# Optimization experiments

Measured on AMD Instinct MI355X. Metric: run time of the kernel, lower is better.

## Reference

```python
import jax, jax.numpy as jnp
import numpy as np

IMG_W, IMG_H = 960.0, 512.0   # image_size (w, h)
HM_W, HM_H = 240, 128         # heatmap_size (w, h)


def _bilinear(fmap, gx, gy):
    # fmap: [C,H,W]; gx, gy: [N] normalized coords; bilinear, align_corners=False, zero padding
    C, H, W = fmap.shape
    ix = (gx + 1.0) * W * 0.5 - 0.5
    iy = (gy + 1.0) * H * 0.5 - 0.5
    x0f = jnp.floor(ix); y0f = jnp.floor(iy)
    wx1 = ix - x0f; wy1 = iy - y0f

    def tap(xf, yf, wgt):
        valid = (xf >= 0) & (xf <= W - 1) & (yf >= 0) & (yf <= H - 1)
        xc = jnp.clip(xf.astype(jnp.int32), 0, W - 1)
        yc = jnp.clip(yf.astype(jnp.int32), 0, H - 1)
        return fmap[:, yc, xc] * (wgt * valid.astype(fmap.dtype))

    return (tap(x0f, y0f, (1 - wx1) * (1 - wy1)) + tap(x0f + 1, y0f, wx1 * (1 - wy1))
            + tap(x0f, y0f + 1, (1 - wx1) * wy1) + tap(x0f + 1, y0f + 1, wx1 * wy1))


def _forward(feature_maps, grid_center, space_center, space_size, sub_space_size,
             cube, centers, trans, cam_R, cam_T, cam_f, cam_c):
    n_cam, B, C, H, W = feature_maps.shape
    vox = jnp.float32(cube)
    fine_n = (space_size / sub_space_size * (vox - 1.0)).astype(jnp.int32) + 1   # [3]
    fine_nf = fine_n.astype(jnp.float32)
    scale = (fine_nf - 1.0) / space_size
    bias = (-sub_space_size / 2.0 / space_size * (fine_nf - 1.0)
            - scale * (space_center - space_size / 2.0))
    centers_tl = jnp.round(grid_center[:, :3] * scale + bias).astype(jnp.int32)  # [B,3]
    offset = (centers_tl.astype(jnp.float32) / (fine_nf - 1.0) * space_size
              - space_size / 2.0 + sub_space_size / 2.0)                          # [B,3]
    mask_xy = jnp.maximum(((1.0 - grid_center[:, 5:7]) / 2.0 * (vox - 1.0)).astype(jnp.int32), 0)
    mask = jnp.concatenate([mask_xy, jnp.zeros((B, 1), jnp.int32)], axis=1)       # [B,3]
    start = jnp.maximum(centers_tl + mask, 0)
    end = jnp.minimum(centers_tl + cube - mask, fine_n)
    end = jnp.maximum(end, start + 1)

    # fixed-size sub-cube of fine-grid indices; out-of-window cells are masked to 0
    v = jnp.arange(cube)
    mesh = jnp.stack(jnp.meshgrid(v, v, v, indexing="ij"), axis=-1).reshape(-1, 3)  # [N,3]
    fidx = centers_tl[:, None, :] + mesh[None]                                       # [B,N,3]
    valid = jnp.all((fidx >= start[:, None, :]) & (fidx < end[:, None, :]), axis=-1)  # [B,N]
    valid = valid & (grid_center[:, 3:4] >= 0)
    world = (space_center - space_size / 2.0
             + fidx.astype(jnp.float32) / (fine_nf - 1.0) * space_size)              # [B,N,3]

    # pinhole world->pixel per (batch, camera)
    rel = world[:, None, :, :] - cam_T[:, :, None, :]                                # [B,K,N,3]
    Xc = jnp.einsum("bkij,bknj->bkni", cam_R, rel)
    xy = cam_f[:, :, None, :] * Xc[..., :2] / Xc[..., 2:3] + cam_c[:, :, None, :]    # [B,K,N,2]
    maxwh = jnp.max(centers * 2.0, axis=-1)[:, :, None, None]
    xy = jnp.clip(xy, -1.0, maxwh)
    xy = jnp.einsum("bkij,bknj->bkni", trans[..., :2], xy) + trans[:, :, None, :, 2]  # affine crop
    xy = xy * jnp.array([HM_W / IMG_W, HM_H / IMG_H], jnp.float32)
    g = jnp.clip(xy / jnp.array([HM_W - 1.0, HM_H - 1.0], jnp.float32) * 2.0 - 1.0, -1.1, 1.1)

    fm = jnp.transpose(feature_maps, (1, 0, 2, 3, 4))                                # [B,K,C,H,W]
    samp = jax.vmap(jax.vmap(_bilinear))(fm, g[..., 0], g[..., 1])                   # [B,K,C,N]
    samp = samp * valid[:, None, None, :].astype(samp.dtype)
    cubes = jnp.sum(samp, axis=1) / (n_cam + 1e-6)            # mean agg (bounding==1)
    cubes = jnp.clip(cubes, 0.0, 1.0).reshape(B, C, cube, cube, cube)
    return cubes, offset


def setup_inputs() -> dict:
    key = jax.random.key(0)
    ks = jax.random.split(key, 10)
    n_cam, B, C, H, W = 5, 4, 15, 128, 240
    feature_maps = jax.random.uniform(ks[0], (n_cam, B, C, H, W), jnp.float32)
    xy = jax.random.uniform(ks[1], (B, 2), minval=-3000.0, maxval=3000.0)
    z = jax.random.uniform(ks[2], (B, 1), minval=800.0, maxval=1200.0)
    flag = jnp.ones((B, 2), jnp.float32)  # cols 3 (validity >= 0) and 4
    m = jax.random.uniform(ks[3], (B, 2), minval=0.6, maxval=1.0)  # cols 5:7 mask fracs
    grid_center = jnp.concatenate([xy, z, flag, m], axis=1)        # [B,7]
    space_center = jnp.array([0.0, 0.0, 1000.0], jnp.float32)
    space_size = jnp.array([8000.0, 8000.0, 2000.0], jnp.float32)
    sub_space_size = jnp.array([2000.0, 2000.0, 2000.0], jnp.float32)
    centers = jnp.array([IMG_W / 2, IMG_H / 2], jnp.float32) + \
        jax.random.uniform(ks[4], (B, n_cam, 2), minval=-5.0, maxval=5.0)
    base = jnp.array([[1.0, 0.0, 0.0], [0.0, 1.0, 0.0]], jnp.float32)
    trans = base + 0.01 * jax.random.normal(ks[5], (B, n_cam, 2, 3), jnp.float32)
    cam_R = jnp.eye(3, dtype=jnp.float32) + 0.05 * jax.random.normal(ks[6], (B, n_cam, 3, 3), jnp.float32)
    t_xy = jax.random.uniform(ks[7], (B, n_cam, 2), minval=-500.0, maxval=500.0)
    cam_T = jnp.concatenate([t_xy, jnp.full((B, n_cam, 1), -6000.0, jnp.float32)], axis=-1)
    cam_f = jax.random.uniform(ks[8], (B, n_cam, 2), minval=500.0, maxval=700.0)
    cam_c = jnp.array([IMG_W / 2, IMG_H / 2], jnp.float32) + \
        jax.random.uniform(ks[9], (B, n_cam, 2), minval=-10.0, maxval=10.0)
    return {"feature_maps": feature_maps, "grid_center": grid_center,
            "space_center": space_center, "space_size": space_size,
            "sub_space_size": sub_space_size, "sub_cube_size": 64,
            "centers": centers, "trans": trans, "cam_R": cam_R,
            "cam_T": cam_T, "cam_f": cam_f, "cam_c": cam_c}


def reference(feature_maps, grid_center, space_center, space_size, sub_space_size,
              sub_cube_size, centers, trans, cam_R, cam_T, cam_f, cam_c):
    return _forward(feature_maps, grid_center, space_center, space_size, sub_space_size,
                    int(sub_cube_size), centers, trans, cam_R, cam_T, cam_f, cam_c)
```

## Files before the change

### kernel.cpp

```cpp
#include <hip/hip_runtime.h>
#include <hip/hip_fp16.h>

#define NCAM 5
#define NC 15
#define NCP 16
#define FH 128
#define FW 240
#define HW (FH*FW)
#define CUBE 64
#define NVOX (CUBE*CUBE*CUBE)
#define MTHREADS 512
#define MBLOCKS_PER_B (NVOX/MTHREADS)
#define TTHREADS 256
#define CSTR 24

__global__ __launch_bounds__(TTHREADS) void transpose_fm(
    const float* __restrict__ fm, __half* __restrict__ fmH,
    const float* __restrict__ gc, const float* __restrict__ space_c,
    const float* __restrict__ space_s, const float* __restrict__ sub_s,
    const float* __restrict__ centers, const float* __restrict__ trans,
    const float* __restrict__ cam_R, const float* __restrict__ cam_T,
    const float* __restrict__ cam_f, const float* __restrict__ cam_c,
    float* __restrict__ camS, int* __restrict__ bwin,
    float* __restrict__ out, int B)
{
    const int t = threadIdx.x;
    if (blockIdx.x == 0 && blockIdx.y == 0) {
        if (t < B) {
            const int b = t;
            #pragma unroll
            for (int d = 0; d < 3; ++d) {
                float ssz = space_s[d], sc = space_c[d], sub = sub_s[d];
                int   fn  = (int)(ssz / sub * (CUBE - 1.0f)) + 1;
                float fnf = (float)fn;
                float scale = (fnf - 1.0f) / ssz;
                float bias  = -sub / 2.0f / ssz * (fnf - 1.0f) - scale * (sc - ssz / 2.0f);
                int ctl = (int)rintf(gc[b*7 + d] * scale + bias);
                int mask = 0;
                if (d < 2) {
                    mask = (int)((1.0f - gc[b*7 + 5 + d]) / 2.0f * (CUBE - 1.0f));
                    if (mask < 0) mask = 0;
                }
                int st = max(ctl + mask, 0);
                int en = min(ctl + CUBE - mask, fn);
                en = max(en, st + 1);
                bwin[b*12 + d]     = ctl;
                bwin[b*12 + 3 + d] = st;
                bwin[b*12 + 6 + d] = en;
                out[(size_t)B * NC * NVOX + b*3 + d] =
                    (float)ctl / (fnf - 1.0f) * ssz - ssz / 2.0f + sub / 2.0f;
            }
            bwin[t*12 + 9] = (gc[t*7 + 3] >= 0.0f) ? 1 : 0;
        }
        if (t < B * NCAM) {
            const int b = t / NCAM, bk = t;
            float sA[3], bA[3];
            #pragma unroll
            for (int d = 0; d < 3; ++d) {
                float ssz = space_s[d], sub = sub_s[d];
                int   fn  = (int)(ssz / sub * (CUBE - 1.0f)) + 1;
                sA[d] = ssz / ((float)fn - 1.0f);
                bA[d] = space_c[d] - ssz * 0.5f;
            }
            const float* R = cam_R + bk*9;
            const float* T = cam_T + bk*3;
            float* P = camS + (size_t)bk * CSTR;
            #pragma unroll
            for (int i = 0; i < 3; ++i) {
                #pragma unroll
                for (int d = 0; d < 3; ++d) P[i*3 + d] = R[i*3 + d] * sA[d];
                P[9 + i] = R[i*3+0]*(bA[0]-T[0]) + R[i*3+1]*(bA[1]-T[1]) + R[i*3+2]*(bA[2]-T[2]);
            }
            P[12] = cam_f[bk*2+0];  P[13] = cam_f[bk*2+1];
            P[14] = cam_c[bk*2+0];  P[15] = cam_c[bk*2+1];
            P[16] = fmaxf(centers[bk*2+0]*2.0f, centers[bk*2+1]*2.0f);
            const float* tr = trans + bk*6;
            const float KX = 60.0f/239.0f, KY = 32.0f/127.0f;
            P[17] = tr[0]*KX;  P[18] = tr[1]*KX;  P[19] = tr[2]*KX - 120.0f;
            P[20] = tr[3]*KY;  P[21] = tr[4]*KY;  P[22] = tr[5]*KY - 64.0f;
            P[23] = 0.0f;
            (void)b;
        }
    }
    const int p  = blockIdx.x * TTHREADS + t;
    const int cb = blockIdx.y;
    const float* src = fm + (size_t)cb * NC * HW + p;
    __half v[NCP];
    #pragma unroll
    for (int c = 0; c < NC; ++c) v[c] = __float2half(src[(size_t)c * HW]);
    v[15] = __float2half(0.0f);
    uint4* dst = (uint4*)(fmH + ((size_t)cb * HW + p) * NCP);
    dst[0] = *(const uint4*)(v);
    dst[1] = *(const uint4*)(v + 8);
}

#define FMA_MIX2(lo, hi, wt, wrd)                                             \
    asm("v_fma_mix_f32 %0, %1, %2, %0 op_sel_hi:[0,1,0]"                      \
        : "+v"(lo) : "v"(wt), "v"(wrd));                                      \
    asm("v_fma_mix_f32 %0, %1, %2, %0 op_sel:[0,1,0] op_sel_hi:[0,1,0]"       \
        : "+v"(hi) : "v"(wt), "v"(wrd));

#define TAPFMA(wt, A, Bv)                                                     \
    FMA_MIX2(acc[0],  acc[1],  wt, A.x)                                       \
    FMA_MIX2(acc[2],  acc[3],  wt, A.y)                                       \
    FMA_MIX2(acc[4],  acc[5],  wt, A.z)                                       \
    FMA_MIX2(acc[6],  acc[7],  wt, A.w)                                       \
    FMA_MIX2(acc[8],  acc[9],  wt, Bv.x)                                      \
    FMA_MIX2(acc[10], acc[11], wt, Bv.y)                                      \
    FMA_MIX2(acc[12], acc[13], wt, Bv.z)                                      \
    FMA_MIX2(acc[14], acc[15], wt, Bv.w)

struct CamProj { unsigned o[4]; float w[4]; };

__device__ __forceinline__ CamProj projcam(const float* __restrict__ P,
                                           float fxf, float fyf, float fzf)
{
    float X0 = fmaf(P[0], fxf, fmaf(P[1], fyf, fmaf(P[2], fzf, P[9])));
    float X1 = fmaf(P[3], fxf, fmaf(P[4], fyf, fmaf(P[5], fzf, P[10])));
    float X2 = fmaf(P[6], fxf, fmaf(P[7], fyf, fmaf(P[8], fzf, P[11])));
    float rz = __builtin_amdgcn_rcpf(X2);
    float mw = P[16];
    float px = fmaf(P[12]*X0, rz, P[14]);
    float py = fmaf(P[13]*X1, rz, P[15]);
    px = fminf(fmaxf(px, -1.0f), mw);
    py = fminf(fmaxf(py, -1.0f), mw);
    float ixf = fminf(fmaxf(fmaf(P[17], px, fmaf(P[18], py, P[19])), -132.0f), 132.0f) + 119.5f;
    float iyf = fminf(fmaxf(fmaf(P[20], px, fmaf(P[21], py, P[22])), -70.4f), 70.4f) + 63.5f;
    float x0f = floorf(ixf), y0f = floorf(iyf);
    float wx1 = ixf - x0f,  wy1 = iyf - y0f;
    float wx0 = 1.0f - wx1, wy0 = 1.0f - wy1;
    int x0 = (int)x0f, y0 = (int)y0f, x1 = x0 + 1, y1 = y0 + 1;
    bool vx0 = (unsigned)x0 <= (FW-1), vx1 = (unsigned)x1 <= (FW-1);
    bool vy0 = (unsigned)y0 <= (FH-1), vy1 = (unsigned)y1 <= (FH-1);
    CamProj r;
    r.w[0] = (vx0 && vy0) ? wx0*wy0 : 0.0f;
    r.w[1] = (vx1 && vy0) ? wx1*wy0 : 0.0f;
    r.w[2] = (vx0 && vy1) ? wx0*wy1 : 0.0f;
    r.w[3] = (vx1 && vy1) ? wx1*wy1 : 0.0f;
    int xc0 = min(max(x0,0),FW-1), xc1 = min(max(x1,0),FW-1);
    int yc0 = min(max(y0,0),FH-1), yc1 = min(max(y1,0),FH-1);
    r.o[0] = (unsigned)(yc0*FW + xc0);  r.o[1] = (unsigned)(yc0*FW + xc1);
    r.o[2] = (unsigned)(yc1*FW + xc0);  r.o[3] = (unsigned)(yc1*FW + xc1);
    return r;
}

__global__ __launch_bounds__(MTHREADS) void proj_main(
    const __half* __restrict__ fmH,
    const float* __restrict__ camS,
    const int* __restrict__ bwin,
    float* __restrict__ out, int B)
{
    const int b = blockIdx.x / MBLOCKS_PER_B;
    const int n = (blockIdx.x % MBLOCKS_PER_B) * MTHREADS + threadIdx.x;
    const int vi = n >> 12, vj = (n >> 6) & 63, vk = n & 63;

    const int* W = bwin + b*12;
    const int fx = W[0] + vi, fy = W[1] + vj, fz = W[2] + vk;
    const bool valid = (fx >= W[3]) & (fx < W[6])
                     & (fy >= W[4]) & (fy < W[7])
                     & (fz >= W[5]) & (fz < W[8])
                     & (W[9] != 0);

    float acc[NCP];
    #pragma unroll
    for (int c = 0; c < NCP; ++c) acc[c] = 0.0f;

    if (valid) {
        const float fxf = (float)fx, fyf = (float)fy, fzf = (float)fz;
        const float* cs = camS + (size_t)(b*NCAM) * CSTR;

        #pragma unroll
        for (int cam = 0; cam < NCAM; ++cam) {
            CamProj cp = projcam(cs + cam*CSTR, fxf, fyf, fzf);
            if (__any((cp.w[0] + cp.w[1] + cp.w[2] + cp.w[3]) != 0.0f)) {
                const __half* bp = fmH + (size_t)(cam*B + b) * HW * NCP;
                const uint4* q0 = (const uint4*)(bp + (size_t)cp.o[0]*NCP);
                const uint4* q1 = (const uint4*)(bp + (size_t)cp.o[1]*NCP);
                const uint4* q2 = (const uint4*)(bp + (size_t)cp.o[2]*NCP);
                const uint4* q3 = (const uint4*)(bp + (size_t)cp.o[3]*NCP);
                uint4 a0 = q0[0], b0 = q0[1];
                uint4 a1 = q1[0], b1 = q1[1];
                uint4 a2 = q2[0], b2 = q2[1];
                uint4 a3 = q3[0], b3 = q3[1];
                TAPFMA(cp.w[0], a0, b0)
                TAPFMA(cp.w[1], a1, b1)
                TAPFMA(cp.w[2], a2, b2)
                TAPFMA(cp.w[3], a3, b3)
            }
        }
    }

    const float RINV = 0.19999996000000800f;
    #pragma unroll
    for (int c = 0; c < NC; ++c) {
        float v = acc[c] * RINV;
        v = fminf(fmaxf(v, 0.0f), 1.0f);
        out[((size_t)(b*NC + c)) * NVOX + n] = v;
    }
}

__global__ __launch_bounds__(256) void proj_fallback(
    const float* __restrict__ fm, const float* __restrict__ gc,
    const float* __restrict__ space_center, const float* __restrict__ space_size,
    const float* __restrict__ sub_size, const float* __restrict__ centers,
    const float* __restrict__ trans, const float* __restrict__ cam_R,
    const float* __restrict__ cam_T, const float* __restrict__ cam_f,
    const float* __restrict__ cam_c, float* __restrict__ out, int B)
{
    const int b = blockIdx.x / (NVOX/256);
    const int n = (blockIdx.x % (NVOX/256)) * 256 + threadIdx.x;
    float ctlf[3], fnf[3], sc[3], ssz[3];
    int   ctl[3], st[3], en[3];
    #pragma unroll
    for (int d = 0; d < 3; ++d) {
        ssz[d] = space_size[d];
        sc[d]  = space_center[d];
        float sub = sub_size[d];
        int fn = (int)(ssz[d] / sub * (CUBE - 1.0f)) + 1;
        fnf[d] = (float)fn;
        float scale = (fnf[d] - 1.0f) / ssz[d];
        float bias  = -sub / 2.0f / ssz[d] * (fnf[d] - 1.0f)
                      - scale * (sc[d] - ssz[d] / 2.0f);
        int c_tl = (int)rintf(gc[b*7 + d] * scale + bias);
        ctl[d]  = c_tl;  ctlf[d] = (float)c_tl;
        int mask = 0;
        if (d < 2) {
            mask = (int)((1.0f - gc[b*7 + 5 + d]) / 2.0f * (CUBE - 1.0f));
            if (mask < 0) mask = 0;
        }
        st[d] = max(c_tl + mask, 0);
        int e = min(c_tl + CUBE - mask, fn);
        en[d] = max(e, st[d] + 1);
    }
    if (n < 3) {
        int d = n;
        out[(size_t)B * NC * NVOX + b*3 + d] =
            ctlf[d] / (fnf[d] - 1.0f) * ssz[d] - ssz[d] / 2.0f + sub_size[d] / 2.0f;
    }
    const int vi = n >> 12, vj = (n >> 6) & 63, vk = n & 63;
    const int fx = ctl[0] + vi, fy = ctl[1] + vj, fz = ctl[2] + vk;
    const bool valid = (fx >= st[0]) & (fx < en[0]) & (fy >= st[1]) & (fy < en[1])
                     & (fz >= st[2]) & (fz < en[2]) & (gc[b*7 + 3] >= 0.0f);
    float acc[NC];
    #pragma unroll
    for (int c = 0; c < NC; ++c) acc[c] = 0.0f;
    if (valid) {
        const float wxw = sc[0] - ssz[0]*0.5f + (float)fx / (fnf[0]-1.0f) * ssz[0];
        const float wyw = sc[1] - ssz[1]*0.5f + (float)fy / (fnf[1]-1.0f) * ssz[1];
        const float wzw = sc[2] - ssz[2]*0.5f + (float)fz / (fnf[2]-1.0f) * ssz[2];
        for (int cam = 0; cam < NCAM; ++cam) {
            const int bk = b*NCAM + cam;
            const float* R = cam_R + bk*9;
            const float* T = cam_T + bk*3;
            float r0 = wxw - T[0], r1 = wyw - T[1], r2 = wzw - T[2];
            float X0 = R[0]*r0 + R[1]*r1 + R[2]*r2;
            float X1 = R[3]*r0 + R[4]*r1 + R[5]*r2;
            float X2 = R[6]*r0 + R[7]*r1 + R[8]*r2;
            float px = cam_f[bk*2+0]*X0/X2 + cam_c[bk*2+0];
            float py = cam_f[bk*2+1]*X1/X2 + cam_c[bk*2+1];
            float maxwh = fmaxf(centers[bk*2+0]*2.0f, centers[bk*2+1]*2.0f);
            px = fminf(fmaxf(px, -1.0f), maxwh);
            py = fminf(fmaxf(py, -1.0f), maxwh);
            const float* tr = trans + bk*6;
            float tx = (tr[0]*px + tr[1]*py + tr[2]) * 0.25f;
            float ty = (tr[3]*px + tr[4]*py + tr[5]) * 0.25f;
            float gx = fminf(fmaxf(tx/239.0f*2.0f - 1.0f, -1.1f), 1.1f);
            float gy = fminf(fmaxf(ty/127.0f*2.0f - 1.0f, -1.1f), 1.1f);
            float ixf = (gx + 1.0f)*(FW*0.5f) - 0.5f;
            float iyf = (gy + 1.0f)*(FH*0.5f) - 0.5f;
            float x0f = floorf(ixf), y0f = floorf(iyf);
            float wx1 = ixf - x0f,  wy1 = iyf - y0f;
            float wx0 = 1.0f - wx1, wy0 = 1.0f - wy1;
            int x0 = (int)x0f, y0 = (int)y0f, x1 = x0 + 1, y1 = y0 + 1;
            bool vx0 = (x0 >= 0) & (x0 <= FW-1), vx1 = (x1 >= 0) & (x1 <= FW-1);
            bool vy0 = (y0 >= 0) & (y0 <= FH-1), vy1 = (y1 >= 0) & (y1 <= FH-1);
            float w00 = wx0*wy0*(float)(vx0 & vy0);
            float w10 = wx1*wy0*(float)(vx1 & vy0);
            float w01 = wx0*wy1*(float)(vx0 & vy1);
            float w11 = wx1*wy1*(float)(vx1 & vy1);
            int xc0 = min(max(x0,0),FW-1), xc1 = min(max(x1,0),FW-1);
            int yc0 = min(max(y0,0),FH-1), yc1 = min(max(y1,0),FH-1);
            int o00 = yc0*FW + xc0, o10 = yc0*FW + xc1;
            int o01 = yc1*FW + xc0, o11 = yc1*FW + xc1;
            const float* base = fm + ((size_t)(cam*B + b)) * NC * HW;
            #pragma unroll
            for (int c = 0; c < NC; ++c) {
                const float* p = base + c*HW;
                acc[c] += w00*p[o00] + w10*p[o10] + w01*p[o01] + w11*p[o11];
            }
        }
    }
    const float invd = (float)(5.0 + 1e-6);
    #pragma unroll
    for (int c = 0; c < NC; ++c) {
        float v = acc[c] / invd;
        v = fminf(fmaxf(v, 0.0f), 1.0f);
        out[((size_t)(b*NC + c)) * NVOX + n] = v;
    }
}

extern "C" void kernel_launch(void* const* d_in, const int* in_sizes, int n_in,
                              void* d_out, int out_size, void* d_ws, size_t ws_size,
                              hipStream_t stream) {
    const float* fm        = (const float*)d_in[0];
    const float* gc        = (const float*)d_in[1];
    const float* space_c   = (const float*)d_in[2];
    const float* space_s   = (const float*)d_in[3];
    const float* sub_s     = (const float*)d_in[4];
    const float* centers   = (const float*)d_in[6];
    const float* trans     = (const float*)d_in[7];
    const float* cam_R     = (const float*)d_in[8];
    const float* cam_T     = (const float*)d_in[9];
    const float* cam_f     = (const float*)d_in[10];
    const float* cam_c     = (const float*)d_in[11];
    float* out = (float*)d_out;
    const int B = in_sizes[1] / 7;

    const size_t FMHB   = (size_t)NCAM * B * HW * NCP * sizeof(__half);
    const size_t CAMOFF = (FMHB + 255) & ~(size_t)255;
    const size_t BWOFF  = (CAMOFF + (size_t)B * NCAM * CSTR * 4 + 255) & ~(size_t)255;
    const size_t NEED   = BWOFF + (size_t)B * 48;

    if (ws_size >= NEED) {
        __half* fmH  = (__half*)d_ws;
        float*  camS = (float*)((char*)d_ws + CAMOFF);
        int*    bwin = (int*)((char*)d_ws + BWOFF);
        dim3 tg(HW / TTHREADS, NCAM * B);
        hipLaunchKernelGGL(transpose_fm, tg, dim3(TTHREADS), 0, stream,
                           fm, fmH, gc, space_c, space_s, sub_s, centers, trans,
                           cam_R, cam_T, cam_f, cam_c, camS, bwin, out, B);
        dim3 grid(B * MBLOCKS_PER_B), block(MTHREADS);
        hipLaunchKernelGGL(proj_main, grid, block, 0, stream,
                           fmH, camS, bwin, out, B);
    } else {
        dim3 grid(B * (NVOX/256)), block(256);
        hipLaunchKernelGGL(proj_fallback, grid, block, 0, stream,
                           fm, gc, space_c, space_s, sub_s,
                           centers, trans, cam_R, cam_T, cam_f, cam_c, out, B);
    }
}
```

Baseline: 45.48 us.

## Remap voxel-to-thread tiling so wavefront lanes span x, transposing output via LDS

Each block now handles one (y, 8-wide z tile) and each wavefront's 64 lanes walk the x axis instead of the contiguous z axis. This is meant to make the bilinear gathers within a wavefront hit nearby feature-map texels and improve cache locality. Results are staged in padded shared memory and transposed so global stores stay coalesced along z, though only in 32-byte runs. The cost is an extra LDS round trip and a block barrier, plus shorter contiguous store segments.

```diff
diff --git a/kernel.cpp b/kernel.cpp
--- a/kernel.cpp
+++ b/kernel.cpp
@@ -9,9 +9,10 @@
 #define HW (FH*FW)
 #define CUBE 64
 #define NVOX (CUBE*CUBE*CUBE)
+#define TTHREADS 256
 #define MTHREADS 512
-#define MBLOCKS_PER_B (NVOX/MTHREADS)
-#define TTHREADS 256
+#define VKB 8
+#define LDSPAD 67
 #define CSTR 24
 
 __global__ __launch_bounds__(TTHREADS) void transpose_fm(
@@ -50,10 +51,10 @@
                 out[(size_t)B * NC * NVOX + b*3 + d] =
                     (float)ctl / (fnf - 1.0f) * ssz - ssz / 2.0f + sub / 2.0f;
             }
-            bwin[t*12 + 9] = (gc[t*7 + 3] >= 0.0f) ? 1 : 0;
+            bwin[b*12 + 9] = (gc[b*7 + 3] >= 0.0f) ? 1 : 0;
         }
         if (t < B * NCAM) {
-            const int b = t / NCAM, bk = t;
+            const int bk = t;
             float sA[3], bA[3];
             #pragma unroll
             for (int d = 0; d < 3; ++d) {
@@ -79,7 +80,6 @@
             P[17] = tr[0]*KX;  P[18] = tr[1]*KX;  P[19] = tr[2]*KX - 120.0f;
             P[20] = tr[3]*KY;  P[21] = tr[4]*KY;  P[22] = tr[5]*KY - 64.0f;
             P[23] = 0.0f;
-            (void)b;
         }
     }
     const int p  = blockIdx.x * TTHREADS + t;
@@ -150,12 +150,19 @@
     const int* __restrict__ bwin,
     float* __restrict__ out, int B)
 {
-    const int b = blockIdx.x / MBLOCKS_PER_B;
-    const int n = (blockIdx.x % MBLOCKS_PER_B) * MTHREADS + threadIdx.x;
-    const int vi = n >> 12, vj = (n >> 6) & 63, vk = n & 63;
+    __shared__ float lds[NC * VKB * LDSPAD];
+    const int bid = blockIdx.x;
+    const int b  = bid >> 9;
+    const int vj = (bid >> 3) & 63;
+    const int kt = bid & 7;
+    const int t  = threadIdx.x;
+    const int l  = t & 63;
+    const int w  = t >> 6;
 
     const int* W = bwin + b*12;
-    const int fx = W[0] + vi, fy = W[1] + vj, fz = W[2] + vk;
+    const int fx = W[0] + l;
+    const int fy = W[1] + vj;
+    const int fz = W[2] + kt*VKB + w;
     const bool valid = (fx >= W[3]) & (fx < W[6])
                      & (fy >= W[4]) & (fy < W[7])
                      & (fz >= W[5]) & (fz < W[8])
@@ -168,7 +175,6 @@
     if (valid) {
         const float fxf = (float)fx, fyf = (float)fy, fzf = (float)fz;
         const float* cs = camS + (size_t)(b*NCAM) * CSTR;
-
         #pragma unroll
         for (int cam = 0; cam < NCAM; ++cam) {
             CamProj cp = projcam(cs + cam*CSTR, fxf, fyf, fzf);
@@ -193,10 +199,17 @@
     const float RINV = 0.19999996000000800f;
     #pragma unroll
     for (int c = 0; c < NC; ++c) {
-        float v = acc[c] * RINV;
-        v = fminf(fmaxf(v, 0.0f), 1.0f);
-        out[((size_t)(b*NC + c)) * NVOX + n] = v;
-    }
+        float v = fminf(fmaxf(acc[c] * RINV, 0.0f), 1.0f);
+        lds[(c*VKB + w)*LDSPAD + l] = v;
+    }
+    __syncthreads();
+
+    const int vi2 = t >> 3, vk2 = t & 7;
+    const size_t base = (size_t)b * NC * NVOX
+                      + (size_t)vi2 * 4096 + vj * 64 + kt * VKB + vk2;
+    #pragma unroll
+    for (int c = 0; c < NC; ++c)
+        out[base + (size_t)c * NVOX] = lds[(c*VKB + vk2)*LDSPAD + vi2];
 }
 
 __global__ __launch_bounds__(256) void proj_fallback(
@@ -329,7 +342,7 @@
         hipLaunchKernelGGL(transpose_fm, tg, dim3(TTHREADS), 0, stream,
                            fm, fmH, gc, space_c, space_s, sub_s, centers, trans,
                            cam_R, cam_T, cam_f, cam_c, camS, bwin, out, B);
-        dim3 grid(B * MBLOCKS_PER_B), block(MTHREADS);
+        dim3 grid(B * 512), block(MTHREADS);
         hipLaunchKernelGGL(proj_main, grid, block, 0, stream,
                            fmH, camS, bwin, out, B);
     } else {
```

Result: slower. 50.92 us (+12.0%).

## Stage per-wave bilinear footprint in LDS before gathering taps

Applied to the files above, without the earlier changes.

Each wavefront uses shuffle reductions to find the bounding box of its bilinear taps for each camera. When the box fits within 256 pixels, the wave loads that patch of the half-precision feature map into LDS once, then reads all four taps from LDS. Otherwise it falls back to direct global gathers. Blocks shrink to 256 threads, the per-camera __any skip is removed, and the 16th padding channel FMA is dropped. The aim is fewer redundant global gathers, at the cost of shuffle-reduction overhead, LDS traffic, and doing projection work even on fully out-of-view cameras.

```diff
diff --git a/kernel.cpp b/kernel.cpp
--- a/kernel.cpp
+++ b/kernel.cpp
@@ -9,10 +9,12 @@
 #define HW (FH*FW)
 #define CUBE 64
 #define NVOX (CUBE*CUBE*CUBE)
-#define MTHREADS 512
-#define MBLOCKS_PER_B (NVOX/MTHREADS)
 #define TTHREADS 256
 #define CSTR 24
+#define CAPPX 256
+#define WBYTES 9216
+
+__device__ __forceinline__ int loff(int s) { return (s << 5) + ((s >> 2) << 4); }
 
 __global__ __launch_bounds__(TTHREADS) void transpose_fm(
     const float* __restrict__ fm, __half* __restrict__ fmH,
@@ -50,10 +52,10 @@
                 out[(size_t)B * NC * NVOX + b*3 + d] =
                     (float)ctl / (fnf - 1.0f) * ssz - ssz / 2.0f + sub / 2.0f;
             }
-            bwin[t*12 + 9] = (gc[t*7 + 3] >= 0.0f) ? 1 : 0;
+            bwin[b*12 + 9] = (gc[b*7 + 3] >= 0.0f) ? 1 : 0;
         }
         if (t < B * NCAM) {
-            const int b = t / NCAM, bk = t;
+            const int bk = t;
             float sA[3], bA[3];
             #pragma unroll
             for (int d = 0; d < 3; ++d) {
@@ -79,7 +81,6 @@
             P[17] = tr[0]*KX;  P[18] = tr[1]*KX;  P[19] = tr[2]*KX - 120.0f;
             P[20] = tr[3]*KY;  P[21] = tr[4]*KY;  P[22] = tr[5]*KY - 64.0f;
             P[23] = 0.0f;
-            (void)b;
         }
     }
     const int p  = blockIdx.x * TTHREADS + t;
@@ -108,93 +109,125 @@
     FMA_MIX2(acc[8],  acc[9],  wt, Bv.x)                                      \
     FMA_MIX2(acc[10], acc[11], wt, Bv.y)                                      \
     FMA_MIX2(acc[12], acc[13], wt, Bv.z)                                      \
-    FMA_MIX2(acc[14], acc[15], wt, Bv.w)
-
-struct CamProj { unsigned o[4]; float w[4]; };
-
-__device__ __forceinline__ CamProj projcam(const float* __restrict__ P,
-                                           float fxf, float fyf, float fzf)
-{
-    float X0 = fmaf(P[0], fxf, fmaf(P[1], fyf, fmaf(P[2], fzf, P[9])));
-    float X1 = fmaf(P[3], fxf, fmaf(P[4], fyf, fmaf(P[5], fzf, P[10])));
-    float X2 = fmaf(P[6], fxf, fmaf(P[7], fyf, fmaf(P[8], fzf, P[11])));
-    float rz = __builtin_amdgcn_rcpf(X2);
-    float mw = P[16];
-    float px = fmaf(P[12]*X0, rz, P[14]);
-    float py = fmaf(P[13]*X1, rz, P[15]);
-    px = fminf(fmaxf(px, -1.0f), mw);
-    py = fminf(fmaxf(py, -1.0f), mw);
-    float ixf = fminf(fmaxf(fmaf(P[17], px, fmaf(P[18], py, P[19])), -132.0f), 132.0f) + 119.5f;
-    float iyf = fminf(fmaxf(fmaf(P[20], px, fmaf(P[21], py, P[22])), -70.4f), 70.4f) + 63.5f;
-    float x0f = floorf(ixf), y0f = floorf(iyf);
-    float wx1 = ixf - x0f,  wy1 = iyf - y0f;
-    float wx0 = 1.0f - wx1, wy0 = 1.0f - wy1;
-    int x0 = (int)x0f, y0 = (int)y0f, x1 = x0 + 1, y1 = y0 + 1;
-    bool vx0 = (unsigned)x0 <= (FW-1), vx1 = (unsigned)x1 <= (FW-1);
-    bool vy0 = (unsigned)y0 <= (FH-1), vy1 = (unsigned)y1 <= (FH-1);
-    CamProj r;
-    r.w[0] = (vx0 && vy0) ? wx0*wy0 : 0.0f;
-    r.w[1] = (vx1 && vy0) ? wx1*wy0 : 0.0f;
-    r.w[2] = (vx0 && vy1) ? wx0*wy1 : 0.0f;
-    r.w[3] = (vx1 && vy1) ? wx1*wy1 : 0.0f;
-    int xc0 = min(max(x0,0),FW-1), xc1 = min(max(x1,0),FW-1);
-    int yc0 = min(max(y0,0),FH-1), yc1 = min(max(y1,0),FH-1);
-    r.o[0] = (unsigned)(yc0*FW + xc0);  r.o[1] = (unsigned)(yc0*FW + xc1);
-    r.o[2] = (unsigned)(yc1*FW + xc0);  r.o[3] = (unsigned)(yc1*FW + xc1);
-    return r;
-}
-
-__global__ __launch_bounds__(MTHREADS) void proj_main(
+    asm("v_fma_mix_f32 %0, %1, %2, %0 op_sel_hi:[0,1,0]"                      \
+        : "+v"(acc[14]) : "v"(wt), "v"(Bv.w));
+
+__global__ __launch_bounds__(TTHREADS) void proj_main(
     const __half* __restrict__ fmH,
     const float* __restrict__ camS,
     const int* __restrict__ bwin,
     float* __restrict__ out, int B)
 {
-    const int b = blockIdx.x / MBLOCKS_PER_B;
-    const int n = (blockIdx.x % MBLOCKS_PER_B) * MTHREADS + threadIdx.x;
-    const int vi = n >> 12, vj = (n >> 6) & 63, vk = n & 63;
-
-    const int* W = bwin + b*12;
-    const int fx = W[0] + vi, fy = W[1] + vj, fz = W[2] + vk;
-    const bool valid = (fx >= W[3]) & (fx < W[6])
-                     & (fy >= W[4]) & (fy < W[7])
-                     & (fz >= W[5]) & (fz < W[8])
-                     & (W[9] != 0);
-
-    float acc[NCP];
-    #pragma unroll
-    for (int c = 0; c < NCP; ++c) acc[c] = 0.0f;
-
-    if (valid) {
+    __shared__ char ldsA[4 * WBYTES];
+    const int t = threadIdx.x, w = t >> 6, l = t & 63;
+    const int bid = blockIdx.x;
+    const int b = bid >> 10, bd = bid & 1023;
+    const int n = bd * 256 + t;
+    const int vi = bd >> 4, vj = (bd * 4 + w) & 63, vk = l;
+
+    const int* Wn = bwin + b*12;
+    const int fx = Wn[0] + vi, fy = Wn[1] + vj, fz = Wn[2] + vk;
+    const bool valid = (fx >= Wn[3]) & (fx < Wn[6])
+                     & (fy >= Wn[4]) & (fy < Wn[7])
+                     & (fz >= Wn[5]) & (fz < Wn[8])
+                     & (Wn[9] != 0);
+    const float validf = valid ? 1.0f : 0.0f;
+
+    float acc[15];
+    #pragma unroll
+    for (int c = 0; c < 15; ++c) acc[c] = 0.0f;
+
+    if (__any(valid)) {
         const float fxf = (float)fx, fyf = (float)fy, fzf = (float)fz;
-        const float* cs = camS + (size_t)(b*NCAM) * CSTR;
-
-        #pragma unroll
+        const float* cs = camS + (size_t)(b * NCAM) * CSTR;
+        char* myl = ldsA + w * WBYTES;
+
         for (int cam = 0; cam < NCAM; ++cam) {
-            CamProj cp = projcam(cs + cam*CSTR, fxf, fyf, fzf);
-            if (__any((cp.w[0] + cp.w[1] + cp.w[2] + cp.w[3]) != 0.0f)) {
-                const __half* bp = fmH + (size_t)(cam*B + b) * HW * NCP;
-                const uint4* q0 = (const uint4*)(bp + (size_t)cp.o[0]*NCP);
-                const uint4* q1 = (const uint4*)(bp + (size_t)cp.o[1]*NCP);
-                const uint4* q2 = (const uint4*)(bp + (size_t)cp.o[2]*NCP);
-                const uint4* q3 = (const uint4*)(bp + (size_t)cp.o[3]*NCP);
-                uint4 a0 = q0[0], b0 = q0[1];
-                uint4 a1 = q1[0], b1 = q1[1];
-                uint4 a2 = q2[0], b2 = q2[1];
-                uint4 a3 = q3[0], b3 = q3[1];
-                TAPFMA(cp.w[0], a0, b0)
-                TAPFMA(cp.w[1], a1, b1)
-                TAPFMA(cp.w[2], a2, b2)
-                TAPFMA(cp.w[3], a3, b3)
-            }
+            const float* P = cs + cam * CSTR;
+            float X0 = fmaf(P[0], fxf, fmaf(P[1], fyf, fmaf(P[2], fzf, P[9])));
+            float X1 = fmaf(P[3], fxf, fmaf(P[4], fyf, fmaf(P[5], fzf, P[10])));
+            float X2 = fmaf(P[6], fxf, fmaf(P[7], fyf, fmaf(P[8], fzf, P[11])));
+            float rz = __builtin_amdgcn_rcpf(X2);
+            float px = fmaf(P[12]*X0, rz, P[14]);
+            float py = fmaf(P[13]*X1, rz, P[15]);
+            float mw = P[16];
+            px = fminf(fmaxf(px, -1.0f), mw);
+            py = fminf(fmaxf(py, -1.0f), mw);
+            float ixf = fminf(fmaxf(fmaf(P[17], px, fmaf(P[18], py, P[19])), -132.0f), 132.0f) + 119.5f;
+            float iyf = fminf(fmaxf(fmaf(P[20], px, fmaf(P[21], py, P[22])), -70.4f), 70.4f) + 63.5f;
+            float x0f = floorf(ixf), y0f = floorf(iyf);
+            float wx1 = ixf - x0f,  wy1 = iyf - y0f;
+            float wx0 = 1.0f - wx1, wy0 = 1.0f - wy1;
+            int x0 = (int)x0f, y0 = (int)y0f, x1 = x0 + 1, y1 = y0 + 1;
+            bool vx0 = (unsigned)x0 <= (FW-1), vx1 = (unsigned)x1 <= (FW-1);
+            bool vy0 = (unsigned)y0 <= (FH-1), vy1 = (unsigned)y1 <= (FH-1);
+            float w0 = ((vx0 && vy0) ? wx0*wy0 : 0.0f) * validf;
+            float w1 = ((vx1 && vy0) ? wx1*wy0 : 0.0f) * validf;
+            float w2 = ((vx0 && vy1) ? wx0*wy1 : 0.0f) * validf;
+            float w3 = ((vx1 && vy1) ? wx1*wy1 : 0.0f) * validf;
+            int xc0 = min(max(x0,0),FW-1), xc1 = min(max(x1,0),FW-1);
+            int yc0 = min(max(y0,0),FH-1), yc1 = min(max(y1,0),FH-1);
+
+            int bx0 = xc0, bx1 = xc1, by0 = yc0, by1 = yc1;
+            #pragma unroll
+            for (int m = 1; m < 64; m <<= 1) {
+                bx0 = min(bx0, __shfl_xor(bx0, m));
+                bx1 = max(bx1, __shfl_xor(bx1, m));
+                by0 = min(by0, __shfl_xor(by0, m));
+                by1 = max(by1, __shfl_xor(by1, m));
+            }
+            int Wd = bx1 - bx0 + 1, Hd = by1 - by0 + 1;
+            int lw = (Wd > 1) ? (32 - __clz(Wd - 1)) : 0;
+            int A  = Hd << lw;
+
+            const __half* bp = fmH + (size_t)(cam*B + b) * HW * NCP;
+            uint4 a0, b0, a1, b1, a2, b2, a3, b3;
+
+            if (A <= CAPPX) {
+                #pragma unroll
+                for (int k = 0; k < 4; ++k) {
+                    int s = l + (k << 6);
+                    if (s < A) {
+                        int spy = by0 + (s >> lw);
+                        int spx = min(bx0 + (s & ((1 << lw) - 1)), FW-1);
+                        const uint4* q = (const uint4*)(bp + (size_t)(spy*FW + spx) * NCP);
+                        uint4 v0 = q[0], v1 = q[1];
+                        char* dp = myl + loff(s);
+                        *(uint4*)dp        = v0;
+                        *(uint4*)(dp + 16) = v1;
+                    }
+                }
+                __asm__ __volatile__("s_waitcnt lgkmcnt(0)" ::: "memory");
+                int dx  = xc1 - xc0;
+                int s00 = ((yc0 - by0) << lw) + (xc0 - bx0);
+                int s01 = ((yc1 - by0) << lw) + (xc0 - bx0);
+                const char* r;
+                r = myl + loff(s00);      a0 = *(const uint4*)r; b0 = *(const uint4*)(r+16);
+                r = myl + loff(s00+dx);   a1 = *(const uint4*)r; b1 = *(const uint4*)(r+16);
+                r = myl + loff(s01);      a2 = *(const uint4*)r; b2 = *(const uint4*)(r+16);
+                r = myl + loff(s01+dx);   a3 = *(const uint4*)r; b3 = *(const uint4*)(r+16);
+            } else {
+                const uint4* q0 = (const uint4*)(bp + (size_t)(yc0*FW + xc0) * NCP);
+                const uint4* q1 = (const uint4*)(bp + (size_t)(yc0*FW + xc1) * NCP);
+                const uint4* q2 = (const uint4*)(bp + (size_t)(yc1*FW + xc0) * NCP);
+                const uint4* q3 = (const uint4*)(bp + (size_t)(yc1*FW + xc1) * NCP);
+                a0 = q0[0]; b0 = q0[1];
+                a1 = q1[0]; b1 = q1[1];
+                a2 = q2[0]; b2 = q2[1];
+                a3 = q3[0]; b3 = q3[1];
+            }
+
+            TAPFMA(w0, a0, b0)
+            TAPFMA(w1, a1, b1)
+            TAPFMA(w2, a2, b2)
+            TAPFMA(w3, a3, b3)
         }
     }
 
     const float RINV = 0.19999996000000800f;
     #pragma unroll
     for (int c = 0; c < NC; ++c) {
-        float v = acc[c] * RINV;
-        v = fminf(fmaxf(v, 0.0f), 1.0f);
+        float v = fminf(fmaxf(acc[c] * RINV, 0.0f), 1.0f);
         out[((size_t)(b*NC + c)) * NVOX + n] = v;
     }
 }
@@ -329,7 +362,7 @@
         hipLaunchKernelGGL(transpose_fm, tg, dim3(TTHREADS), 0, stream,
                            fm, fmH, gc, space_c, space_s, sub_s, centers, trans,
                            cam_R, cam_T, cam_f, cam_c, camS, bwin, out, B);
-        dim3 grid(B * MBLOCKS_PER_B), block(MTHREADS);
+        dim3 grid(B * 1024), block(TTHREADS);
         hipLaunchKernelGGL(proj_main, grid, block, 0, stream,
                            fmH, camS, bwin, out, B);
     } else {
```

New measurement: 54.37 us. 1.2x slower.

## Remap workgroups across XCDs, shrink blocks, drop wave-skip branch and padding FMA

Applied to the files above, without the earlier changes.

Remaps the main kernel's block index so consecutive voxel blocks land on the same XCD. Neighbouring voxels, which sample nearby feature-map texels, then share that XCD's L2. Block size drops from 512 to 256 threads. The per-camera __any early-out branch is removed, and the accumulation skips the unused 16th padding channel FMA. Loads are now issued unconditionally for every camera, which may cost extra memory traffic where a camera misses the voxel entirely.

```diff
diff --git a/kernel.cpp b/kernel.cpp
--- a/kernel.cpp
+++ b/kernel.cpp
@@ -9,9 +9,8 @@
 #define HW (FH*FW)
 #define CUBE 64
 #define NVOX (CUBE*CUBE*CUBE)
-#define MTHREADS 512
-#define MBLOCKS_PER_B (NVOX/MTHREADS)
 #define TTHREADS 256
+#define MTHREADS 256
 #define CSTR 24
 
 __global__ __launch_bounds__(TTHREADS) void transpose_fm(
@@ -50,10 +49,10 @@
                 out[(size_t)B * NC * NVOX + b*3 + d] =
                     (float)ctl / (fnf - 1.0f) * ssz - ssz / 2.0f + sub / 2.0f;
             }
-            bwin[t*12 + 9] = (gc[t*7 + 3] >= 0.0f) ? 1 : 0;
+            bwin[b*12 + 9] = (gc[b*7 + 3] >= 0.0f) ? 1 : 0;
         }
         if (t < B * NCAM) {
-            const int b = t / NCAM, bk = t;
+            const int bk = t;
             float sA[3], bA[3];
             #pragma unroll
             for (int d = 0; d < 3; ++d) {
@@ -79,7 +78,6 @@
             P[17] = tr[0]*KX;  P[18] = tr[1]*KX;  P[19] = tr[2]*KX - 120.0f;
             P[20] = tr[3]*KY;  P[21] = tr[4]*KY;  P[22] = tr[5]*KY - 64.0f;
             P[23] = 0.0f;
-            (void)b;
         }
     }
     const int p  = blockIdx.x * TTHREADS + t;
@@ -108,41 +106,8 @@
     FMA_MIX2(acc[8],  acc[9],  wt, Bv.x)                                      \
     FMA_MIX2(acc[10], acc[11], wt, Bv.y)                                      \
     FMA_MIX2(acc[12], acc[13], wt, Bv.z)                                      \
-    FMA_MIX2(acc[14], acc[15], wt, Bv.w)
-
-struct CamProj { unsigned o[4]; float w[4]; };
-
-__device__ __forceinline__ CamProj projcam(const float* __restrict__ P,
-                                           float fxf, float fyf, float fzf)
-{
-    float X0 = fmaf(P[0], fxf, fmaf(P[1], fyf, fmaf(P[2], fzf, P[9])));
-    float X1 = fmaf(P[3], fxf, fmaf(P[4], fyf, fmaf(P[5], fzf, P[10])));
-    float X2 = fmaf(P[6], fxf, fmaf(P[7], fyf, fmaf(P[8], fzf, P[11])));
-    float rz = __builtin_amdgcn_rcpf(X2);
-    float mw = P[16];
-    float px = fmaf(P[12]*X0, rz, P[14]);
-    float py = fmaf(P[13]*X1, rz, P[15]);
-    px = fminf(fmaxf(px, -1.0f), mw);
-    py = fminf(fmaxf(py, -1.0f), mw);
-    float ixf = fminf(fmaxf(fmaf(P[17], px, fmaf(P[18], py, P[19])), -132.0f), 132.0f) + 119.5f;
-    float iyf = fminf(fmaxf(fmaf(P[20], px, fmaf(P[21], py, P[22])), -70.4f), 70.4f) + 63.5f;
-    float x0f = floorf(ixf), y0f = floorf(iyf);
-    float wx1 = ixf - x0f,  wy1 = iyf - y0f;
-    float wx0 = 1.0f - wx1, wy0 = 1.0f - wy1;
-    int x0 = (int)x0f, y0 = (int)y0f, x1 = x0 + 1, y1 = y0 + 1;
-    bool vx0 = (unsigned)x0 <= (FW-1), vx1 = (unsigned)x1 <= (FW-1);
-    bool vy0 = (unsigned)y0 <= (FH-1), vy1 = (unsigned)y1 <= (FH-1);
-    CamProj r;
-    r.w[0] = (vx0 && vy0) ? wx0*wy0 : 0.0f;
-    r.w[1] = (vx1 && vy0) ? wx1*wy0 : 0.0f;
-    r.w[2] = (vx0 && vy1) ? wx0*wy1 : 0.0f;
-    r.w[3] = (vx1 && vy1) ? wx1*wy1 : 0.0f;
-    int xc0 = min(max(x0,0),FW-1), xc1 = min(max(x1,0),FW-1);
-    int yc0 = min(max(y0,0),FH-1), yc1 = min(max(y1,0),FH-1);
-    r.o[0] = (unsigned)(yc0*FW + xc0);  r.o[1] = (unsigned)(yc0*FW + xc1);
-    r.o[2] = (unsigned)(yc1*FW + xc0);  r.o[3] = (unsigned)(yc1*FW + xc1);
-    return r;
-}
+    asm("v_fma_mix_f32 %0, %1, %2, %0 op_sel_hi:[0,1,0]"                      \
+        : "+v"(acc[14]) : "v"(wt), "v"(Bv.w));
 
 __global__ __launch_bounds__(MTHREADS) void proj_main(
     const __half* __restrict__ fmH,
@@ -150,8 +115,13 @@
     const int* __restrict__ bwin,
     float* __restrict__ out, int B)
 {
-    const int b = blockIdx.x / MBLOCKS_PER_B;
-    const int n = (blockIdx.x % MBLOCKS_PER_B) * MTHREADS + threadIdx.x;
+    const unsigned nwg = gridDim.x;
+    const unsigned q = nwg >> 3, r = nwg & 7;
+    const unsigned xcd = blockIdx.x & 7, idx = blockIdx.x >> 3;
+    const unsigned wgid = (xcd < r ? xcd * (q + 1) : r * (q + 1) + (xcd - r) * q) + idx;
+
+    const int b = wgid >> 10;
+    const int n = (int)(wgid & 1023) * MTHREADS + threadIdx.x;
     const int vi = n >> 12, vj = (n >> 6) & 63, vk = n & 63;
 
     const int* W = bwin + b*12;
@@ -161,40 +131,62 @@
                      & (fz >= W[5]) & (fz < W[8])
                      & (W[9] != 0);
 
-    float acc[NCP];
-    #pragma unroll
-    for (int c = 0; c < NCP; ++c) acc[c] = 0.0f;
+    float acc[15];
+    #pragma unroll
+    for (int c = 0; c < 15; ++c) acc[c] = 0.0f;
 
     if (valid) {
         const float fxf = (float)fx, fyf = (float)fy, fzf = (float)fz;
-        const float* cs = camS + (size_t)(b*NCAM) * CSTR;
+        const float* cs = camS + (size_t)(b * NCAM) * CSTR;
 
         #pragma unroll
         for (int cam = 0; cam < NCAM; ++cam) {
-            CamProj cp = projcam(cs + cam*CSTR, fxf, fyf, fzf);
-            if (__any((cp.w[0] + cp.w[1] + cp.w[2] + cp.w[3]) != 0.0f)) {
-                const __half* bp = fmH + (size_t)(cam*B + b) * HW * NCP;
-                const uint4* q0 = (const uint4*)(bp + (size_t)cp.o[0]*NCP);
-                const uint4* q1 = (const uint4*)(bp + (size_t)cp.o[1]*NCP);
-                const uint4* q2 = (const uint4*)(bp + (size_t)cp.o[2]*NCP);
-                const uint4* q3 = (const uint4*)(bp + (size_t)cp.o[3]*NCP);
-                uint4 a0 = q0[0], b0 = q0[1];
-                uint4 a1 = q1[0], b1 = q1[1];
-                uint4 a2 = q2[0], b2 = q2[1];
-                uint4 a3 = q3[0], b3 = q3[1];
-                TAPFMA(cp.w[0], a0, b0)
-                TAPFMA(cp.w[1], a1, b1)
-                TAPFMA(cp.w[2], a2, b2)
-                TAPFMA(cp.w[3], a3, b3)
-            }
+            const float* P = cs + cam * CSTR;
+            float X0 = fmaf(P[0], fxf, fmaf(P[1], fyf, fmaf(P[2], fzf, P[9])));
+            float X1 = fmaf(P[3], fxf, fmaf(P[4], fyf, fmaf(P[5], fzf, P[10])));
+            float X2 = fmaf(P[6], fxf, fmaf(P[7], fyf, fmaf(P[8], fzf, P[11])));
+            float rz = __builtin_amdgcn_rcpf(X2);
+            float px = fmaf(P[12]*X0, rz, P[14]);
+            float py = fmaf(P[13]*X1, rz, P[15]);
+            float mw = P[16];
+            px = fminf(fmaxf(px, -1.0f), mw);
+            py = fminf(fmaxf(py, -1.0f), mw);
+            float ixf = fminf(fmaxf(fmaf(P[17], px, fmaf(P[18], py, P[19])), -132.0f), 132.0f) + 119.5f;
+            float iyf = fminf(fmaxf(fmaf(P[20], px, fmaf(P[21], py, P[22])), -70.4f), 70.4f) + 63.5f;
+            float x0f = floorf(ixf), y0f = floorf(iyf);
+            float wx1 = ixf - x0f,  wy1 = iyf - y0f;
+            float wx0 = 1.0f - wx1, wy0 = 1.0f - wy1;
+            int x0 = (int)x0f, y0 = (int)y0f, x1 = x0 + 1, y1 = y0 + 1;
+            bool vx0 = (unsigned)x0 <= (FW-1), vx1 = (unsigned)x1 <= (FW-1);
+            bool vy0 = (unsigned)y0 <= (FH-1), vy1 = (unsigned)y1 <= (FH-1);
+            float w0 = (vx0 && vy0) ? wx0*wy0 : 0.0f;
+            float w1 = (vx1 && vy0) ? wx1*wy0 : 0.0f;
+            float w2 = (vx0 && vy1) ? wx0*wy1 : 0.0f;
+            float w3 = (vx1 && vy1) ? wx1*wy1 : 0.0f;
+            int xc0 = min(max(x0,0),FW-1), xc1 = min(max(x1,0),FW-1);
+            int yc0 = min(max(y0,0),FH-1), yc1 = min(max(y1,0),FH-1);
+
+            const __half* bp = fmH + (size_t)(cam*B + b) * HW * NCP;
+            const uint4* q0 = (const uint4*)(bp + (size_t)(yc0*FW + xc0) * NCP);
+            const uint4* q1 = (const uint4*)(bp + (size_t)(yc0*FW + xc1) * NCP);
+            const uint4* q2 = (const uint4*)(bp + (size_t)(yc1*FW + xc0) * NCP);
+            const uint4* q3 = (const uint4*)(bp + (size_t)(yc1*FW + xc1) * NCP);
+            uint4 a0 = q0[0], b0 = q0[1];
+            uint4 a1 = q1[0], b1 = q1[1];
+            uint4 a2 = q2[0], b2 = q2[1];
+            uint4 a3 = q3[0], b3 = q3[1];
+
+            TAPFMA(w0, a0, b0)
+            TAPFMA(w1, a1, b1)
+            TAPFMA(w2, a2, b2)
+            TAPFMA(w3, a3, b3)
         }
     }
 
     const float RINV = 0.19999996000000800f;
     #pragma unroll
     for (int c = 0; c < NC; ++c) {
-        float v = acc[c] * RINV;
-        v = fminf(fmaxf(v, 0.0f), 1.0f);
+        float v = fminf(fmaxf(acc[c] * RINV, 0.0f), 1.0f);
         out[((size_t)(b*NC + c)) * NVOX + n] = v;
     }
 }
@@ -329,7 +321,7 @@
         hipLaunchKernelGGL(transpose_fm, tg, dim3(TTHREADS), 0, stream,
                            fm, fmH, gc, space_c, space_s, sub_s, centers, trans,
                            cam_R, cam_T, cam_f, cam_c, camS, bwin, out, B);
-        dim3 grid(B * MBLOCKS_PER_B), block(MTHREADS);
+        dim3 grid(B * 1024), block(MTHREADS);
         hipLaunchKernelGGL(proj_main, grid, block, 0, stream,
                            fmH, camS, bwin, out, B);
     } else {
```

Measured after the change: 40.07 us. -11.9%, faster.
